# Kernel tuning notes

Measured on AMD Instinct MI355X. Metric: run time of the kernel, lower is better.

Reference implementation:

```python
import jax, jax.numpy as jnp
import numpy as np
import math

H = 8  # num_heads

def setup_inputs() -> dict:
    key = jax.random.key(0)
    ks = jax.random.split(key, 12)
    B, N, M, k = 2, 8192, 8192, 32
    dq, dk, dv = 256, 256, 256
    s = 1.0 / math.sqrt(dq)
    inp = {
        'Q': jax.random.normal(ks[0], (B, N, dq), dtype=jnp.float32),
        'K': jax.random.normal(ks[1], (B, M, dk), dtype=jnp.float32),
        'neighbours': jax.random.randint(ks[2], (B, N, k), 0, M),
        'Wq': jax.random.normal(ks[3], (dq, dv), dtype=jnp.float32) * s,
        'bq': jnp.zeros((dv,), dtype=jnp.float32),
        'Wk': jax.random.normal(ks[4], (dk, dv), dtype=jnp.float32) * s,
        'bk': jnp.zeros((dv,), dtype=jnp.float32),
        'Wv': jax.random.normal(ks[5], (dk, dv), dtype=jnp.float32) * s,
        'bv': jnp.zeros((dv,), dtype=jnp.float32),
        'Wo': jax.random.normal(ks[6], (dv, dv), dtype=jnp.float32) * (1.0 / math.sqrt(dv)),
        'bo': jnp.zeros((dv,), dtype=jnp.float32),
    }
    return inp

def reference(Q, K, neighbours, Wq, bq, Wk, bk, Wv, bv, Wo, bo):
    B, N, _ = Q.shape
    dv = Wq.shape[1]
    ds = dv // H
    # project and split heads (contiguous channel chunks == reshape)
    Qh = (Q @ Wq + bq).reshape(B, N, H, ds)            # [B,N,H,ds]
    Kh = (K @ Wk + bk).reshape(B, -1, H, ds)           # [B,M,H,ds]
    Vh = (K @ Wv + bv).reshape(B, -1, H, ds)           # [B,M,H,ds]
    # gather per-node kNN neighbour keys/values: [B,N,k,H,ds]
    gather = jax.vmap(lambda x, idx: x[idx])
    Kn = gather(Kh, neighbours)
    Vn = gather(Vh, neighbours)
    # scale uses full latent size (faithful to original), not head dim
    scale = 1.0 / math.sqrt(dv)
    E = jnp.einsum('bnhd,bnkhd->bnhk', Qh, Kn) * scale  # [B,N,H,k]
    A = jax.nn.softmax(E, axis=-1)
    AV = jnp.einsum('bnhk,bnkhd->bnhd', A, Vn).reshape(B, N, dv)
    return AV @ Wo + bo
```

## Files before the change

kernel.cpp:

```cpp
#include <hip/hip_runtime.h>
#include <stdint.h>

typedef unsigned short u16;
typedef __attribute__((ext_vector_type(8))) short short8;
typedef __attribute__((ext_vector_type(4))) float f32x4;

__device__ __forceinline__ float bf2f(u16 u) {
    union { unsigned int i; float f; } v;
    v.i = ((unsigned int)u) << 16;
    return v.f;
}
__device__ __forceinline__ u16 f2bf(float f) {
    union { float f; unsigned int i; } v; v.f = f;
    unsigned int b = v.i;
    return (u16)((b + 0x7FFFu + ((b >> 16) & 1u)) >> 16);
}

typedef const __attribute__((address_space(1))) void* as1cv;
typedef __attribute__((address_space(3))) void* as3v;
__device__ __forceinline__ void gload16(const void* g, void* l) {
    __builtin_amdgcn_global_load_lds((as1cv)g, (as3v)l, 16, 0, 0);
}

__global__ __launch_bounds__(256) void cvt(
    const float* __restrict__ Q, const float* __restrict__ K,
    u16* __restrict__ Qb, u16* __restrict__ Kb)
{
    const float* src = blockIdx.y ? K : Q;
    u16* dst = blockIdx.y ? Kb : Qb;
    size_t i = ((size_t)blockIdx.x * 256 + threadIdx.x) * 8;
    float4 a = *reinterpret_cast<const float4*>(src + i);
    float4 b = *reinterpret_cast<const float4*>(src + i + 4);
    u16 o[8] = {f2bf(a.x), f2bf(a.y), f2bf(a.z), f2bf(a.w),
                f2bf(b.x), f2bf(b.y), f2bf(b.z), f2bf(b.w)};
    *reinterpret_cast<uint4*>(dst + i) = *reinterpret_cast<const uint4*>(o);
}

__global__ __launch_bounds__(256) void wprep(
    const float* __restrict__ W0, const float* __restrict__ W1,
    const float* __restrict__ W2, const float* __restrict__ W3,
    u16* __restrict__ T0, u16* __restrict__ T1,
    u16* __restrict__ T2, u16* __restrict__ T3)
{
    const float* W = blockIdx.z == 0 ? W0 : blockIdx.z == 1 ? W1 : blockIdx.z == 2 ? W2 : W3;
    u16*        T  = blockIdx.z == 0 ? T0 : blockIdx.z == 1 ? T1 : blockIdx.z == 2 ? T2 : T3;
    __shared__ u16 ts[64][65];
    int k0 = blockIdx.x * 64, n0 = blockIdx.y * 64;
    int t = threadIdx.x;
    int r = t >> 2, cq = (t & 3) * 16;
    const float4* src = reinterpret_cast<const float4*>(W + (k0 + r) * 256 + n0 + cq);
    for (int u = 0; u < 4; ++u) {
        float4 v = src[u];
        int c = cq + u * 4;
        ts[r][c + 0] = f2bf(v.x); ts[r][c + 1] = f2bf(v.y);
        ts[r][c + 2] = f2bf(v.z); ts[r][c + 3] = f2bf(v.w);
    }
    __syncthreads();
    u16* dst = T + (n0 + r) * 256 + k0 + cq;
    for (int u = 0; u < 16; ++u) dst[u] = ts[cq + u][r];
}

template <bool F32OUT>
__device__ __forceinline__ void gemm_core(
    const u16* __restrict__ Ab, const u16* __restrict__ Wt,
    const float* __restrict__ bias, void* __restrict__ Cv,
    int row0, int col0)
{
    __shared__ u16 As[128 * 64];
    __shared__ u16 Bs[128 * 64];

    int t = threadIdx.x;
    int lane = t & 63, w = t >> 6;
    int wr = (w >> 1) * 64, wc = (w & 1) * 64;
    int qd = lane >> 4, md = lane & 15;

    int srow = w * 32 + (lane >> 3);
    int scol = (lane & 7) * 8;

    f32x4 acc[4][4] = {};

    for (int kt = 0; kt < 256; kt += 64) {
#pragma unroll
        for (int u = 0; u < 4; ++u) {
            int r = srow + u * 8;
            gload16(Ab + (size_t)(row0 + r) * 256 + kt + scol,
                    (char*)As + (w * 4 + u) * 1024);
            gload16(Wt + (size_t)(col0 + r) * 256 + kt + scol,
                    (char*)Bs + (w * 4 + u) * 1024);
        }
        __syncthreads();
#pragma unroll
        for (int ks = 0; ks < 64; ks += 32) {
            short8 af[4], bf[4];
#pragma unroll
            for (int i = 0; i < 4; ++i)
                af[i] = *reinterpret_cast<const short8*>(
                    &As[(wr + i * 16 + md) * 64 + ks + qd * 8]);
#pragma unroll
            for (int j = 0; j < 4; ++j)
                bf[j] = *reinterpret_cast<const short8*>(
                    &Bs[(wc + j * 16 + md) * 64 + ks + qd * 8]);
#pragma unroll
            for (int i = 0; i < 4; ++i)
#pragma unroll
                for (int j = 0; j < 4; ++j)
                    acc[i][j] = __builtin_amdgcn_mfma_f32_16x16x32_bf16(
                        af[i], bf[j], acc[i][j], 0, 0, 0);
        }
        __syncthreads();
    }

#pragma unroll
    for (int i = 0; i < 4; ++i)
#pragma unroll
        for (int j = 0; j < 4; ++j) {
            int col = col0 + wc + j * 16 + md;
            float b = bias[col];
#pragma unroll
            for (int r = 0; r < 4; ++r) {
                int row = row0 + wr + i * 16 + qd * 4 + r;
                if (F32OUT)
                    ((float*)Cv)[(size_t)row * 256 + col] = acc[i][j][r] + b;
                else
                    ((u16*)Cv)[(size_t)row * 256 + col] = f2bf(acc[i][j][r] + b);
            }
        }
}

__global__ __launch_bounds__(256) void gemm_proj(
    const u16* __restrict__ Qb, const u16* __restrict__ Kb,
    const u16* __restrict__ Wtq, const u16* __restrict__ Wtk, const u16* __restrict__ Wtv,
    const float* __restrict__ bq, const float* __restrict__ bk, const float* __restrict__ bv,
    u16* __restrict__ Qh, u16* __restrict__ Kh, u16* __restrict__ Vh)
{
    int z = blockIdx.z;
    const u16*   A    = (z == 0) ? Qb  : Kb;
    const u16*   Wt   = (z == 0) ? Wtq : (z == 1) ? Wtk : Wtv;
    const float* bias = (z == 0) ? bq  : (z == 1) ? bk  : bv;
    u16*         C    = (z == 0) ? Qh  : (z == 1) ? Kh  : Vh;
    gemm_core<false>(A, Wt, bias, C, blockIdx.x * 128, blockIdx.y * 128);
}

__global__ __launch_bounds__(256) void gemm_out(
    const u16* __restrict__ A, const u16* __restrict__ Wt,
    const float* __restrict__ bias, float* __restrict__ Cout)
{
    gemm_core<true>(A, Wt, bias, Cout, blockIdx.x * 128, blockIdx.y * 128);
}

__global__ __launch_bounds__(256) void attn(
    const u16* __restrict__ Qh, const u16* __restrict__ Kh, const u16* __restrict__ Vh,
    const int* __restrict__ nbr, u16* __restrict__ AVb)
{
    __shared__ u16 Ks[32][264];
    __shared__ float qs[256];
    __shared__ float as_[256];
    __shared__ int ji[32];

    int t = threadIdx.x;
    int row = blockIdx.x;
    int b = row >> 13;
    size_t qbase = (size_t)row * 256;

    qs[t] = bf2f(Qh[qbase + t]);
    if (t < 32) ji[t] = nbr[(size_t)row * 32 + t];
    __syncthreads();

    {
        int j = t >> 3, seg = t & 7;
        size_t kb = (((size_t)b << 13) + (size_t)ji[j]) * 256;
        const uint4* ksrc = reinterpret_cast<const uint4*>(Kh + kb);
        uint4* kdst = reinterpret_cast<uint4*>(&Ks[j][seg * 32]);
        kdst[0] = ksrc[seg * 4 + 0]; kdst[1] = ksrc[seg * 4 + 1];
        kdst[2] = ksrc[seg * 4 + 2]; kdst[3] = ksrc[seg * 4 + 3];
    }
    __syncthreads();

    int h = t >> 5, j = t & 31;
    float e = 0.f;
#pragma unroll
    for (int c = 0; c < 4; ++c) {
        short8 kv = *reinterpret_cast<const short8*>(&Ks[j][h * 32 + c * 8]);
#pragma unroll
        for (int u = 0; u < 8; ++u)
            e += qs[h * 32 + c * 8 + u] * bf2f((u16)kv[u]);
    }
    e *= 0.0625f;

    float m = e;
    for (int off = 16; off; off >>= 1) m = fmaxf(m, __shfl_xor(m, off, 32));
    float p = __expf(e - m);
    float s = p;
    for (int off = 16; off; off >>= 1) s += __shfl_xor(s, off, 32);
    as_[t] = p / s;
    __syncthreads();

    int hh = t >> 5;
    float acc = 0.f;
    size_t vbase = ((size_t)b << 13) * 256;
#pragma unroll
    for (int jj = 0; jj < 32; ++jj) {
        float wgt = as_[hh * 32 + jj];
        acc += wgt * bf2f(Vh[vbase + (size_t)ji[jj] * 256 + t]);
    }
    AVb[qbase + t] = f2bf(acc);
}

extern "C" void kernel_launch(void* const* d_in, const int* in_sizes, int n_in,
                              void* d_out, int out_size, void* d_ws, size_t ws_size,
                              hipStream_t stream) {
    const float* Q   = (const float*)d_in[0];
    const float* K   = (const float*)d_in[1];
    const int*   nbr = (const int*)d_in[2];
    const float* Wq  = (const float*)d_in[3];
    const float* bq  = (const float*)d_in[4];
    const float* Wk  = (const float*)d_in[5];
    const float* bk  = (const float*)d_in[6];
    const float* Wv  = (const float*)d_in[7];
    const float* bv  = (const float*)d_in[8];
    const float* Wo  = (const float*)d_in[9];
    const float* bo  = (const float*)d_in[10];
    float* out = (float*)d_out;

    char* ws = (char*)d_ws;
    size_t off = 0;
    auto alloc = [&](size_t bytes) -> void* {
        void* p = ws + off;
        off += (bytes + 255) & ~(size_t)255;
        return p;
    };
    const size_t MN = 16384;
    u16* Wtq = (u16*)alloc(256 * 256 * 2);
    u16* Wtk = (u16*)alloc(256 * 256 * 2);
    u16* Wtv = (u16*)alloc(256 * 256 * 2);
    u16* Wto = (u16*)alloc(256 * 256 * 2);
    u16* Qb  = (u16*)alloc(MN * 256 * 2);
    u16* Kb  = (u16*)alloc(MN * 256 * 2);
    u16* Qh  = (u16*)alloc(MN * 256 * 2);
    u16* Kh  = (u16*)alloc(MN * 256 * 2);
    u16* Vh  = (u16*)alloc(MN * 256 * 2);
    u16* AVb = (u16*)alloc(MN * 256 * 2);

    cvt<<<dim3(2048, 2), 256, 0, stream>>>(Q, K, Qb, Kb);
    wprep<<<dim3(4, 4, 4), 256, 0, stream>>>(Wq, Wk, Wv, Wo, Wtq, Wtk, Wtv, Wto);
    gemm_proj<<<dim3(128, 2, 3), 256, 0, stream>>>(Qb, Kb, Wtq, Wtk, Wtv,
                                                   bq, bk, bv, Qh, Kh, Vh);
    attn<<<dim3(16384), 256, 0, stream>>>(Qh, Kh, Vh, nbr, AVb);
    gemm_out<<<dim3(128, 2, 1), 256, 0, stream>>>(AVb, Wto, bo, out);
}
```

Baseline: 166.5 us.

## Merge prep kernels and restructure attention to two rows per block with direct gathers

Fuses the fp32-to-bf16 conversion and the weight transpose into one launch. The attention kernel now handles two query rows per block and drops the LDS staging of neighbour keys. Each thread reads its head's key slice straight from global memory, and value gathers use 4-byte loads that each cover two channels. This is meant to cut launch overhead, LDS traffic and barriers, and to widen the memory accesses. In exchange, key reads become less coalesced gathers.

```diff
diff --git a/kernel.cpp b/kernel.cpp
--- a/kernel.cpp
+++ b/kernel.cpp
@@ -22,31 +22,34 @@
     __builtin_amdgcn_global_load_lds((as1cv)g, (as3v)l, 16, 0, 0);
 }
 
-__global__ __launch_bounds__(256) void cvt(
+__global__ __launch_bounds__(256) void prep(
     const float* __restrict__ Q, const float* __restrict__ K,
-    u16* __restrict__ Qb, u16* __restrict__ Kb)
-{
-    const float* src = blockIdx.y ? K : Q;
-    u16* dst = blockIdx.y ? Kb : Qb;
-    size_t i = ((size_t)blockIdx.x * 256 + threadIdx.x) * 8;
-    float4 a = *reinterpret_cast<const float4*>(src + i);
-    float4 b = *reinterpret_cast<const float4*>(src + i + 4);
-    u16 o[8] = {f2bf(a.x), f2bf(a.y), f2bf(a.z), f2bf(a.w),
-                f2bf(b.x), f2bf(b.y), f2bf(b.z), f2bf(b.w)};
-    *reinterpret_cast<uint4*>(dst + i) = *reinterpret_cast<const uint4*>(o);
-}
-
-__global__ __launch_bounds__(256) void wprep(
-    const float* __restrict__ W0, const float* __restrict__ W1,
-    const float* __restrict__ W2, const float* __restrict__ W3,
-    u16* __restrict__ T0, u16* __restrict__ T1,
-    u16* __restrict__ T2, u16* __restrict__ T3)
-{
-    const float* W = blockIdx.z == 0 ? W0 : blockIdx.z == 1 ? W1 : blockIdx.z == 2 ? W2 : W3;
-    u16*        T  = blockIdx.z == 0 ? T0 : blockIdx.z == 1 ? T1 : blockIdx.z == 2 ? T2 : T3;
+    const float* __restrict__ Wq, const float* __restrict__ Wk,
+    const float* __restrict__ Wv, const float* __restrict__ Wo,
+    u16* __restrict__ Qb, u16* __restrict__ Kb,
+    u16* __restrict__ Tq, u16* __restrict__ Tk,
+    u16* __restrict__ Tv, u16* __restrict__ To)
+{
     __shared__ u16 ts[64][65];
-    int k0 = blockIdx.x * 64, n0 = blockIdx.y * 64;
+    int bi = blockIdx.x;
     int t = threadIdx.x;
+    if (bi < 4096) {
+        const float* src = (bi < 2048) ? Q : K;
+        u16* dst = (bi < 2048) ? Qb : Kb;
+        int blk = bi & 2047;
+        size_t i = ((size_t)blk * 256 + t) * 8;
+        float4 a = *reinterpret_cast<const float4*>(src + i);
+        float4 b = *reinterpret_cast<const float4*>(src + i + 4);
+        u16 o[8] = {f2bf(a.x), f2bf(a.y), f2bf(a.z), f2bf(a.w),
+                    f2bf(b.x), f2bf(b.y), f2bf(b.z), f2bf(b.w)};
+        *reinterpret_cast<uint4*>(dst + i) = *reinterpret_cast<const uint4*>(o);
+        return;
+    }
+    int wi = bi - 4096;
+    int wsel = wi >> 4;
+    const float* W = wsel == 0 ? Wq : wsel == 1 ? Wk : wsel == 2 ? Wv : Wo;
+    u16*        T  = wsel == 0 ? Tq : wsel == 1 ? Tk : wsel == 2 ? Tv : To;
+    int k0 = ((wi >> 2) & 3) * 64, n0 = (wi & 3) * 64;
     int r = t >> 2, cq = (t & 3) * 16;
     const float4* src = reinterpret_cast<const float4*>(W + (k0 + r) * 256 + n0 + cq);
     for (int u = 0; u < 4; ++u) {
@@ -152,58 +155,77 @@
     const u16* __restrict__ Qh, const u16* __restrict__ Kh, const u16* __restrict__ Vh,
     const int* __restrict__ nbr, u16* __restrict__ AVb)
 {
-    __shared__ u16 Ks[32][264];
-    __shared__ float qs[256];
-    __shared__ float as_[256];
-    __shared__ int ji[32];
+    __shared__ float qs[2][256];
+    __shared__ float as_[2][256];
+    __shared__ int jb[2][32];
 
     int t = threadIdx.x;
-    int row = blockIdx.x;
-    int b = row >> 13;
-    size_t qbase = (size_t)row * 256;
-
-    qs[t] = bf2f(Qh[qbase + t]);
-    if (t < 32) ji[t] = nbr[(size_t)row * 32 + t];
+    int row0 = blockIdx.x * 2;
+    int b = row0 >> 13;
+
+    {
+        int r = t >> 7, c = (t & 127) * 2;
+        unsigned int v = *reinterpret_cast<const unsigned int*>(
+            Qh + (size_t)(row0 + r) * 256 + c);
+        union { unsigned int i; float f; } lo, hi;
+        lo.i = v << 16; hi.i = v & 0xffff0000u;
+        qs[r][c] = lo.f; qs[r][c + 1] = hi.f;
+    }
+    if (t < 64) {
+        int r = t >> 5, j = t & 31;
+        int ji = nbr[(size_t)(row0 + r) * 32 + j];
+        jb[r][j] = ((b << 13) + ji) << 9;
+    }
     __syncthreads();
 
+    int h = t >> 5, j = t & 31;
+#pragma unroll
+    for (int r = 0; r < 2; ++r) {
+        const char* kp = (const char*)Kh + jb[r][j] + h * 64;
+        uint4 kw[4];
+        kw[0] = *reinterpret_cast<const uint4*>(kp);
+        kw[1] = *reinterpret_cast<const uint4*>(kp + 16);
+        kw[2] = *reinterpret_cast<const uint4*>(kp + 32);
+        kw[3] = *reinterpret_cast<const uint4*>(kp + 48);
+        const float* q = &qs[r][h * 32];
+        float e = 0.f;
+#pragma unroll
+        for (int cq4 = 0; cq4 < 4; ++cq4) {
+            unsigned int wds[4] = {kw[cq4].x, kw[cq4].y, kw[cq4].z, kw[cq4].w};
+#pragma unroll
+            for (int u = 0; u < 4; ++u) {
+                union { unsigned int i; float f; } lo, hi;
+                lo.i = wds[u] << 16; hi.i = wds[u] & 0xffff0000u;
+                e += q[cq4 * 8 + u * 2] * lo.f + q[cq4 * 8 + u * 2 + 1] * hi.f;
+            }
+        }
+        e *= 0.0625f;
+        float m = e;
+        for (int off = 16; off; off >>= 1) m = fmaxf(m, __shfl_xor(m, off, 32));
+        float p = __expf(e - m);
+        float s = p;
+        for (int off = 16; off; off >>= 1) s += __shfl_xor(s, off, 32);
+        as_[r][t] = p / s;
+    }
+    __syncthreads();
+
     {
-        int j = t >> 3, seg = t & 7;
-        size_t kb = (((size_t)b << 13) + (size_t)ji[j]) * 256;
-        const uint4* ksrc = reinterpret_cast<const uint4*>(Kh + kb);
-        uint4* kdst = reinterpret_cast<uint4*>(&Ks[j][seg * 32]);
-        kdst[0] = ksrc[seg * 4 + 0]; kdst[1] = ksrc[seg * 4 + 1];
-        kdst[2] = ksrc[seg * 4 + 2]; kdst[3] = ksrc[seg * 4 + 3];
-    }
-    __syncthreads();
-
-    int h = t >> 5, j = t & 31;
-    float e = 0.f;
-#pragma unroll
-    for (int c = 0; c < 4; ++c) {
-        short8 kv = *reinterpret_cast<const short8*>(&Ks[j][h * 32 + c * 8]);
-#pragma unroll
-        for (int u = 0; u < 8; ++u)
-            e += qs[h * 32 + c * 8 + u] * bf2f((u16)kv[u]);
-    }
-    e *= 0.0625f;
-
-    float m = e;
-    for (int off = 16; off; off >>= 1) m = fmaxf(m, __shfl_xor(m, off, 32));
-    float p = __expf(e - m);
-    float s = p;
-    for (int off = 16; off; off >>= 1) s += __shfl_xor(s, off, 32);
-    as_[t] = p / s;
-    __syncthreads();
-
-    int hh = t >> 5;
-    float acc = 0.f;
-    size_t vbase = ((size_t)b << 13) * 256;
-#pragma unroll
-    for (int jj = 0; jj < 32; ++jj) {
-        float wgt = as_[hh * 32 + jj];
-        acc += wgt * bf2f(Vh[vbase + (size_t)ji[jj] * 256 + t]);
-    }
-    AVb[qbase + t] = f2bf(acc);
+        int r = t >> 7, c = t & 127, hh = c >> 4;
+        const float* aw = &as_[r][hh * 32];
+        float a0 = 0.f, a1 = 0.f;
+#pragma unroll
+        for (int jj = 0; jj < 32; ++jj) {
+            unsigned int v = *reinterpret_cast<const unsigned int*>(
+                (const char*)Vh + jb[r][jj] + c * 4);
+            union { unsigned int i; float f; } lo, hi;
+            lo.i = v << 16; hi.i = v & 0xffff0000u;
+            float wgt = aw[jj];
+            a0 += wgt * lo.f; a1 += wgt * hi.f;
+        }
+        u16 o[2] = {f2bf(a0), f2bf(a1)};
+        *reinterpret_cast<unsigned int*>(AVb + (size_t)(row0 + r) * 256 + c * 2) =
+            *reinterpret_cast<const unsigned int*>(o);
+    }
 }
 
 extern "C" void kernel_launch(void* const* d_in, const int* in_sizes, int n_in,
@@ -241,10 +263,10 @@
     u16* Vh  = (u16*)alloc(MN * 256 * 2);
     u16* AVb = (u16*)alloc(MN * 256 * 2);
 
-    cvt<<<dim3(2048, 2), 256, 0, stream>>>(Q, K, Qb, Kb);
-    wprep<<<dim3(4, 4, 4), 256, 0, stream>>>(Wq, Wk, Wv, Wo, Wtq, Wtk, Wtv, Wto);
+    prep<<<dim3(4160), 256, 0, stream>>>(Q, K, Wq, Wk, Wv, Wo,
+                                         Qb, Kb, Wtq, Wtk, Wtv, Wto);
     gemm_proj<<<dim3(128, 2, 3), 256, 0, stream>>>(Qb, Kb, Wtq, Wtk, Wtv,
                                                    bq, bk, bv, Qh, Kh, Vh);
-    attn<<<dim3(16384), 256, 0, stream>>>(Qh, Kh, Vh, nbr, AVb);
+    attn<<<dim3(8192), 256, 0, stream>>>(Qh, Kh, Vh, nbr, AVb);
     gemm_out<<<dim3(128, 2, 1), 256, 0, stream>>>(AVb, Wto, bo, out);
 }
```

Measured after the change: 168.2 us. About the same (+1.0%).
